# Kernel tuning notes

Measured on AMD Instinct MI355X. Metric: run time of the kernel, lower is better.

## Reference

```python
import jax, jax.numpy as jnp
import numpy as np

N = 50000   # nodes
E = 600000  # edges (avg degree 12)
D = 128     # embedding dim (hardcoded in original: np.zeros(128))
P = 5       # propagation iterations (self.p)


def setup_inputs() -> dict:
    key = jax.random.key(0)
    ks = jax.random.split(key, 10)
    x = jax.random.normal(ks[0], (N, D), jnp.float32)
    g = jax.random.normal(ks[1], (D,), jnp.float32)
    dist = jax.random.uniform(ks[2], (E,), jnp.float32)
    w1 = jax.random.normal(ks[3], (1,), jnp.float32)
    w2 = jax.random.normal(ks[4], (1,), jnp.float32)
    w3 = jax.random.normal(ks[5], (1,), jnp.float32)
    w4 = jax.random.normal(ks[6], (1,), jnp.float32)
    w5 = jax.random.normal(ks[7], (1,), jnp.float32)
    src = jax.random.randint(ks[8], (E,), 0, N)
    dst = jax.random.randint(ks[9], (E,), 0, N)
    return {"x": x, "g": g, "dist": dist, "w1": w1, "w2": w2, "w3": w3,
            "w4": w4, "w5": w5, "src": src, "dst": dst}


def reference(x, g, dist, w1, w2, w3, w4, w5, src, dst):
    # travel_times[i] = sum_{j in N(i)} w5 * dist(i,j)  -- iteration-invariant
    travel = jax.ops.segment_sum(w5[0] * dist, src, num_segments=N)  # [N]
    # per-node affine part, constant across the P iterations
    base = w1[0] * x + w2[0] * g[None, :] + w4[0] * jax.nn.relu(travel)[:, None]  # [N, D]
    u = x  # new_u_vect starts as a copy of x
    for _ in range(P):
        # u_sum[i] = sum_{j in N(i)} u[j]  (gather + segment-sum, synchronous update)
        u_sum = jax.ops.segment_sum(u[dst], src, num_segments=N)  # [N, D]
        u = base + w3[0] * u_sum
    return jax.nn.relu(u)
```

## Files before the change

kernel.cpp:

```cpp
#include <hip/hip_runtime.h>

#define D 128
#define D4 32
#define CAPH 32

typedef float v4f __attribute__((ext_vector_type(4)));
typedef _Float16 h4 __attribute__((ext_vector_type(4)));

static inline size_t align_up(size_t v, size_t a) { return (v + a - 1) & ~(a - 1); }

__global__ void fill_ell_kernel(const int* __restrict__ src,
                                const int* __restrict__ dst,
                                const float* __restrict__ dist,
                                unsigned long long* __restrict__ packedA,
                                unsigned long long* __restrict__ packedB,
                                unsigned short* __restrict__ adjA,
                                unsigned short* __restrict__ adjB,
                                int E, int Ehalf) {
  int e = blockIdx.x * blockDim.x + threadIdx.x;
  if (e >= E) return;
  int s = src[e];
  unsigned long long fx = (unsigned long long)(dist[e] * 4294967296.0f);
  unsigned long long val = (1ull << 48) | fx;
  if (e < Ehalf) {
    unsigned long long old = atomicAdd(&packedA[s], val);
    unsigned int slot = (unsigned int)(old >> 48);
    if (slot < CAPH) adjA[(size_t)s * CAPH + slot] = (unsigned short)dst[e];
  } else {
    unsigned long long old = atomicAdd(&packedB[s], val);
    unsigned int slot = (unsigned int)(old >> 48);
    if (slot < CAPH) adjB[(size_t)s * CAPH + slot] = (unsigned short)dst[e];
  }
}

__global__ void base_seed_kernel(const v4f* __restrict__ x4, const v4f* __restrict__ g4,
                                 const unsigned long long* __restrict__ packedA,
                                 const unsigned long long* __restrict__ packedB,
                                 const float* __restrict__ w1p, const float* __restrict__ w2p,
                                 const float* __restrict__ w4p, const float* __restrict__ w5p,
                                 h4* __restrict__ base, h4* __restrict__ uA,
                                 h4* __restrict__ uB, int n) {
  int i = blockIdx.x * blockDim.x + threadIdx.x;
  int node = i >> 5;
  int lane = i & 31;
  if (node > n) return;
  size_t idx = (size_t)i;
  if (node == n) {
    h4 z = {0, 0, 0, 0};
    uA[idx] = z;
    uB[idx] = z;
    return;
  }
  v4f xv = x4[(size_t)node * D4 + lane];
  v4f gv = g4[lane];
  unsigned long long sum = (packedA[node] & 0xFFFFFFFFFFFFull)
                         + (packedB[node] & 0xFFFFFFFFFFFFull);
  float ds = (float)sum * (1.0f / 4294967296.0f);
  float t = w5p[0] * ds;
  t = t > 0.f ? t : 0.f;
  v4f b = w1p[0] * xv + w2p[0] * gv;
  b += t * w4p[0];
  base[idx] = __builtin_convertvector(b, h4);
  uA[idx] = __builtin_convertvector(xv, h4);
}

__global__ __launch_bounds__(256) void prop_kernel(
    const h4* __restrict__ uin, const h4* __restrict__ base,
    const unsigned long long* __restrict__ packedA,
    const unsigned long long* __restrict__ packedB,
    const unsigned short* __restrict__ adjA,
    const unsigned short* __restrict__ adjB,
    const float* __restrict__ w3p,
    void* __restrict__ uout, int n, int final_relu)
{
  int half  = blockIdx.x & 1;
  int chunk = blockIdx.x >> 1;
  int group = threadIdx.x >> 4;
  int lane  = threadIdx.x & 15;
  int node  = chunk * 16 + group;
  if (node >= n) return;

  unsigned long long pA = packedA[node];
  unsigned long long pB = packedB[node];
  int degA = (int)(pA >> 48); if (degA > CAPH) degA = CAPH;
  int degB = (int)(pB >> 48); if (degB > CAPH) degB = CAPH;

  const unsigned short* rowA = adjA + (size_t)node * CAPH;
  const unsigned short* rowB = adjB + (size_t)node * CAPH;
  int a0 = rowA[lane];
  int a1 = rowA[lane + 16];
  int b0 = rowB[lane];
  int b1 = rowB[lane + 16];

  const h4* uh = uin + (size_t)half * 16 + lane;

  v4f acc0 = {0.f,0.f,0.f,0.f}, acc1 = acc0, acc2 = acc0, acc3 = acc0;

  for (int k = 0; k < degA; k += 8) {
    int sel = (k >= 16) ? a1 : a0;
    int j0 = __shfl(sel, (k + 0) & 15, 16); j0 = (k + 0 < degA) ? j0 : n;
    int j1 = __shfl(sel, (k + 1) & 15, 16); j1 = (k + 1 < degA) ? j1 : n;
    int j2 = __shfl(sel, (k + 2) & 15, 16); j2 = (k + 2 < degA) ? j2 : n;
    int j3 = __shfl(sel, (k + 3) & 15, 16); j3 = (k + 3 < degA) ? j3 : n;
    int j4 = __shfl(sel, (k + 4) & 15, 16); j4 = (k + 4 < degA) ? j4 : n;
    int j5 = __shfl(sel, (k + 5) & 15, 16); j5 = (k + 5 < degA) ? j5 : n;
    int j6 = __shfl(sel, (k + 6) & 15, 16); j6 = (k + 6 < degA) ? j6 : n;
    int j7 = __shfl(sel, (k + 7) & 15, 16); j7 = (k + 7 < degA) ? j7 : n;
    h4 v0 = uh[(size_t)j0 * 32];
    h4 v1 = uh[(size_t)j1 * 32];
    h4 v2 = uh[(size_t)j2 * 32];
    h4 v3 = uh[(size_t)j3 * 32];
    h4 v4 = uh[(size_t)j4 * 32];
    h4 v5 = uh[(size_t)j5 * 32];
    h4 v6 = uh[(size_t)j6 * 32];
    h4 v7 = uh[(size_t)j7 * 32];
    acc0 += __builtin_convertvector(v0, v4f) + __builtin_convertvector(v1, v4f);
    acc1 += __builtin_convertvector(v2, v4f) + __builtin_convertvector(v3, v4f);
    acc2 += __builtin_convertvector(v4, v4f) + __builtin_convertvector(v5, v4f);
    acc3 += __builtin_convertvector(v6, v4f) + __builtin_convertvector(v7, v4f);
  }
  for (int k = 0; k < degB; k += 8) {
    int sel = (k >= 16) ? b1 : b0;
    int j0 = __shfl(sel, (k + 0) & 15, 16); j0 = (k + 0 < degB) ? j0 : n;
    int j1 = __shfl(sel, (k + 1) & 15, 16); j1 = (k + 1 < degB) ? j1 : n;
    int j2 = __shfl(sel, (k + 2) & 15, 16); j2 = (k + 2 < degB) ? j2 : n;
    int j3 = __shfl(sel, (k + 3) & 15, 16); j3 = (k + 3 < degB) ? j3 : n;
    int j4 = __shfl(sel, (k + 4) & 15, 16); j4 = (k + 4 < degB) ? j4 : n;
    int j5 = __shfl(sel, (k + 5) & 15, 16); j5 = (k + 5 < degB) ? j5 : n;
    int j6 = __shfl(sel, (k + 6) & 15, 16); j6 = (k + 6 < degB) ? j6 : n;
    int j7 = __shfl(sel, (k + 7) & 15, 16); j7 = (k + 7 < degB) ? j7 : n;
    h4 v0 = uh[(size_t)j0 * 32];
    h4 v1 = uh[(size_t)j1 * 32];
    h4 v2 = uh[(size_t)j2 * 32];
    h4 v3 = uh[(size_t)j3 * 32];
    h4 v4 = uh[(size_t)j4 * 32];
    h4 v5 = uh[(size_t)j5 * 32];
    h4 v6 = uh[(size_t)j6 * 32];
    h4 v7 = uh[(size_t)j7 * 32];
    acc0 += __builtin_convertvector(v0, v4f) + __builtin_convertvector(v1, v4f);
    acc1 += __builtin_convertvector(v2, v4f) + __builtin_convertvector(v3, v4f);
    acc2 += __builtin_convertvector(v4, v4f) + __builtin_convertvector(v5, v4f);
    acc3 += __builtin_convertvector(v6, v4f) + __builtin_convertvector(v7, v4f);
  }
  v4f asum = (acc0 + acc1) + (acc2 + acc3);

  size_t idx = (size_t)node * 32 + half * 16 + lane;
  v4f bb = __builtin_convertvector(base[idx], v4f);
  v4f r = bb + w3p[0] * asum;

  if (final_relu) {
    r.x = r.x > 0.f ? r.x : 0.f;
    r.y = r.y > 0.f ? r.y : 0.f;
    r.z = r.z > 0.f ? r.z : 0.f;
    r.w = r.w > 0.f ? r.w : 0.f;
    __builtin_nontemporal_store(r, (v4f*)uout + idx);
  } else {
    ((h4*)uout)[idx] = __builtin_convertvector(r, h4);
  }
}

extern "C" void kernel_launch(void* const* d_in, const int* in_sizes, int n_in,
                              void* d_out, int out_size, void* d_ws, size_t ws_size,
                              hipStream_t stream) {
  const float* x    = (const float*)d_in[0];
  const float* g    = (const float*)d_in[1];
  const float* dist = (const float*)d_in[2];
  const float* w1   = (const float*)d_in[3];
  const float* w2   = (const float*)d_in[4];
  const float* w3   = (const float*)d_in[5];
  const float* w4   = (const float*)d_in[6];
  const float* w5   = (const float*)d_in[7];
  const int*   src  = (const int*)d_in[8];
  const int*   dst  = (const int*)d_in[9];

  const int N = in_sizes[0] / D;
  const int E = in_sizes[2];
  const int Ehalf = E / 2;

  char* ws = (char*)d_ws;
  size_t o = 0;
  unsigned long long* packedA = (unsigned long long*)(ws + o); o += align_up((size_t)N * 8, 256);
  unsigned long long* packedB = (unsigned long long*)(ws + o);
  size_t zero_end = o + (size_t)N * 8;
  o += align_up((size_t)N * 8, 256);
  unsigned short* adjA = (unsigned short*)(ws + o); o += align_up((size_t)N * CAPH * 2, 256);
  unsigned short* adjB = (unsigned short*)(ws + o); o += align_up((size_t)N * CAPH * 2, 256);
  h4* baseB = (h4*)(ws + o); o += align_up((size_t)(N + 1) * D * 2, 256);
  h4* uA    = (h4*)(ws + o); o += align_up((size_t)(N + 1) * D * 2, 256);
  h4* uB    = (h4*)(ws + o); o += align_up((size_t)(N + 1) * D * 2, 256);
  float* out = (float*)d_out;

  hipMemsetAsync(ws, 0, zero_end, stream);

  const int tb = 256;
  const int eblocks = (E + tb - 1) / tb;
  const int sthreads = (N + 1) * 32;
  const int sblocks = (sthreads + tb - 1) / tb;

  fill_ell_kernel<<<eblocks, tb, 0, stream>>>(src, dst, dist, packedA, packedB,
                                              adjA, adjB, E, Ehalf);
  base_seed_kernel<<<sblocks, tb, 0, stream>>>((const v4f*)x, (const v4f*)g,
                                               packedA, packedB,
                                               w1, w2, w4, w5, baseB, uA, uB, N);

  const int chunks = (N + 15) / 16;
  const int pblocks = chunks * 2;
  prop_kernel<<<pblocks, 256, 0, stream>>>(uA, baseB, packedA, packedB, adjA, adjB, w3, uB,  N, 0);
  prop_kernel<<<pblocks, 256, 0, stream>>>(uB, baseB, packedA, packedB, adjA, adjB, w3, uA,  N, 0);
  prop_kernel<<<pblocks, 256, 0, stream>>>(uA, baseB, packedA, packedB, adjA, adjB, w3, uB,  N, 0);
  prop_kernel<<<pblocks, 256, 0, stream>>>(uB, baseB, packedA, packedB, adjA, adjB, w3, uA,  N, 0);
  prop_kernel<<<pblocks, 256, 0, stream>>>(uA, baseB, packedA, packedB, adjA, adjB, w3, out, N, 1);
}
```

Measured before the change: 254.3 us.

## Split fp16 node features into four column-quarter planes for gather locality

Stores u and base as four separate planes of 32 columns (64 bytes per node per plane) instead of row-major, and has each block handle one quarter for 32 nodes with 8 lanes per node. Each gather now touches a smaller contiguous slice, and each plane's working set is a quarter of the full array, so it may stay in cache across the blocks that share a quarter. The first 8 neighbors of both edge halves are also peeled into one batch of 16 independent loads to raise memory-level parallelism. The risk is that 64-byte gather segments underuse cache lines, and four times as many blocks each re-read adjacency and degree data.

```diff
diff --git a/kernel.cpp b/kernel.cpp
--- a/kernel.cpp
+++ b/kernel.cpp
@@ -42,17 +42,19 @@
                                  h4* __restrict__ uB, int n) {
   int i = blockIdx.x * blockDim.x + threadIdx.x;
   int node = i >> 5;
-  int lane = i & 31;
+  int l = i & 31;
   if (node > n) return;
-  size_t idx = (size_t)i;
+  int q  = l >> 3;
+  int lq = l & 7;
+  size_t po = ((size_t)q * (n + 1) + node) * 8 + lq;
   if (node == n) {
     h4 z = {0, 0, 0, 0};
-    uA[idx] = z;
-    uB[idx] = z;
+    uA[po] = z;
+    uB[po] = z;
     return;
   }
-  v4f xv = x4[(size_t)node * D4 + lane];
-  v4f gv = g4[lane];
+  v4f xv = x4[(size_t)node * D4 + l];
+  v4f gv = g4[l];
   unsigned long long sum = (packedA[node] & 0xFFFFFFFFFFFFull)
                          + (packedB[node] & 0xFFFFFFFFFFFFull);
   float ds = (float)sum * (1.0f / 4294967296.0f);
@@ -60,8 +62,8 @@
   t = t > 0.f ? t : 0.f;
   v4f b = w1p[0] * xv + w2p[0] * gv;
   b += t * w4p[0];
-  base[idx] = __builtin_convertvector(b, h4);
-  uA[idx] = __builtin_convertvector(xv, h4);
+  base[po] = __builtin_convertvector(b, h4);
+  uA[po]   = __builtin_convertvector(xv, h4);
 }
 
 __global__ __launch_bounds__(256) void prop_kernel(
@@ -73,11 +75,11 @@
     const float* __restrict__ w3p,
     void* __restrict__ uout, int n, int final_relu)
 {
-  int half  = blockIdx.x & 1;
-  int chunk = blockIdx.x >> 1;
-  int group = threadIdx.x >> 4;
-  int lane  = threadIdx.x & 15;
-  int node  = chunk * 16 + group;
+  int q     = blockIdx.x & 3;
+  int chunk = blockIdx.x >> 2;
+  int group = threadIdx.x >> 3;
+  int lane  = threadIdx.x & 7;
+  int node  = chunk * 32 + group;
   if (node >= n) return;
 
   unsigned long long pA = packedA[node];
@@ -88,64 +90,111 @@
   const unsigned short* rowA = adjA + (size_t)node * CAPH;
   const unsigned short* rowB = adjB + (size_t)node * CAPH;
   int a0 = rowA[lane];
-  int a1 = rowA[lane + 16];
+  int a1 = rowA[lane + 8];
+  int a2 = rowA[lane + 16];
+  int a3 = rowA[lane + 24];
   int b0 = rowB[lane];
-  int b1 = rowB[lane + 16];
-
-  const h4* uh = uin + (size_t)half * 16 + lane;
+  int b1 = rowB[lane + 8];
+  int b2 = rowB[lane + 16];
+  int b3 = rowB[lane + 24];
+
+  const h4* uq = uin + ((size_t)q * (n + 1)) * 8 + lane;
+  size_t po = ((size_t)q * (n + 1) + node) * 8 + lane;
+  v4f bb = __builtin_convertvector(base[po], v4f);
 
   v4f acc0 = {0.f,0.f,0.f,0.f}, acc1 = acc0, acc2 = acc0, acc3 = acc0;
 
-  for (int k = 0; k < degA; k += 8) {
-    int sel = (k >= 16) ? a1 : a0;
-    int j0 = __shfl(sel, (k + 0) & 15, 16); j0 = (k + 0 < degA) ? j0 : n;
-    int j1 = __shfl(sel, (k + 1) & 15, 16); j1 = (k + 1 < degA) ? j1 : n;
-    int j2 = __shfl(sel, (k + 2) & 15, 16); j2 = (k + 2 < degA) ? j2 : n;
-    int j3 = __shfl(sel, (k + 3) & 15, 16); j3 = (k + 3 < degA) ? j3 : n;
-    int j4 = __shfl(sel, (k + 4) & 15, 16); j4 = (k + 4 < degA) ? j4 : n;
-    int j5 = __shfl(sel, (k + 5) & 15, 16); j5 = (k + 5 < degA) ? j5 : n;
-    int j6 = __shfl(sel, (k + 6) & 15, 16); j6 = (k + 6 < degA) ? j6 : n;
-    int j7 = __shfl(sel, (k + 7) & 15, 16); j7 = (k + 7 < degA) ? j7 : n;
-    h4 v0 = uh[(size_t)j0 * 32];
-    h4 v1 = uh[(size_t)j1 * 32];
-    h4 v2 = uh[(size_t)j2 * 32];
-    h4 v3 = uh[(size_t)j3 * 32];
-    h4 v4 = uh[(size_t)j4 * 32];
-    h4 v5 = uh[(size_t)j5 * 32];
-    h4 v6 = uh[(size_t)j6 * 32];
-    h4 v7 = uh[(size_t)j7 * 32];
+  {
+    int jA0 = __shfl(a0, 0, 8); jA0 = (0 < degA) ? jA0 : n;
+    int jA1 = __shfl(a0, 1, 8); jA1 = (1 < degA) ? jA1 : n;
+    int jA2 = __shfl(a0, 2, 8); jA2 = (2 < degA) ? jA2 : n;
+    int jA3 = __shfl(a0, 3, 8); jA3 = (3 < degA) ? jA3 : n;
+    int jA4 = __shfl(a0, 4, 8); jA4 = (4 < degA) ? jA4 : n;
+    int jA5 = __shfl(a0, 5, 8); jA5 = (5 < degA) ? jA5 : n;
+    int jA6 = __shfl(a0, 6, 8); jA6 = (6 < degA) ? jA6 : n;
+    int jA7 = __shfl(a0, 7, 8); jA7 = (7 < degA) ? jA7 : n;
+    int jB0 = __shfl(b0, 0, 8); jB0 = (0 < degB) ? jB0 : n;
+    int jB1 = __shfl(b0, 1, 8); jB1 = (1 < degB) ? jB1 : n;
+    int jB2 = __shfl(b0, 2, 8); jB2 = (2 < degB) ? jB2 : n;
+    int jB3 = __shfl(b0, 3, 8); jB3 = (3 < degB) ? jB3 : n;
+    int jB4 = __shfl(b0, 4, 8); jB4 = (4 < degB) ? jB4 : n;
+    int jB5 = __shfl(b0, 5, 8); jB5 = (5 < degB) ? jB5 : n;
+    int jB6 = __shfl(b0, 6, 8); jB6 = (6 < degB) ? jB6 : n;
+    int jB7 = __shfl(b0, 7, 8); jB7 = (7 < degB) ? jB7 : n;
+    h4 vA0 = uq[(size_t)jA0 * 8];
+    h4 vA1 = uq[(size_t)jA1 * 8];
+    h4 vA2 = uq[(size_t)jA2 * 8];
+    h4 vA3 = uq[(size_t)jA3 * 8];
+    h4 vA4 = uq[(size_t)jA4 * 8];
+    h4 vA5 = uq[(size_t)jA5 * 8];
+    h4 vA6 = uq[(size_t)jA6 * 8];
+    h4 vA7 = uq[(size_t)jA7 * 8];
+    h4 vB0 = uq[(size_t)jB0 * 8];
+    h4 vB1 = uq[(size_t)jB1 * 8];
+    h4 vB2 = uq[(size_t)jB2 * 8];
+    h4 vB3 = uq[(size_t)jB3 * 8];
+    h4 vB4 = uq[(size_t)jB4 * 8];
+    h4 vB5 = uq[(size_t)jB5 * 8];
+    h4 vB6 = uq[(size_t)jB6 * 8];
+    h4 vB7 = uq[(size_t)jB7 * 8];
+    acc0 += __builtin_convertvector(vA0, v4f) + __builtin_convertvector(vA1, v4f);
+    acc1 += __builtin_convertvector(vA2, v4f) + __builtin_convertvector(vA3, v4f);
+    acc2 += __builtin_convertvector(vA4, v4f) + __builtin_convertvector(vA5, v4f);
+    acc3 += __builtin_convertvector(vA6, v4f) + __builtin_convertvector(vA7, v4f);
+    acc0 += __builtin_convertvector(vB0, v4f) + __builtin_convertvector(vB1, v4f);
+    acc1 += __builtin_convertvector(vB2, v4f) + __builtin_convertvector(vB3, v4f);
+    acc2 += __builtin_convertvector(vB4, v4f) + __builtin_convertvector(vB5, v4f);
+    acc3 += __builtin_convertvector(vB6, v4f) + __builtin_convertvector(vB7, v4f);
+  }
+
+  for (int k = 8; k < degA; k += 8) {
+    int sel = (k >= 24) ? a3 : (k >= 16) ? a2 : a1;
+    int j0 = __shfl(sel, 0, 8); j0 = (k + 0 < degA) ? j0 : n;
+    int j1 = __shfl(sel, 1, 8); j1 = (k + 1 < degA) ? j1 : n;
+    int j2 = __shfl(sel, 2, 8); j2 = (k + 2 < degA) ? j2 : n;
+    int j3 = __shfl(sel, 3, 8); j3 = (k + 3 < degA) ? j3 : n;
+    int j4 = __shfl(sel, 4, 8); j4 = (k + 4 < degA) ? j4 : n;
+    int j5 = __shfl(sel, 5, 8); j5 = (k + 5 < degA) ? j5 : n;
+    int j6 = __shfl(sel, 6, 8); j6 = (k + 6 < degA) ? j6 : n;
+    int j7 = __shfl(sel, 7, 8); j7 = (k + 7 < degA) ? j7 : n;
+    h4 v0 = uq[(size_t)j0 * 8];
+    h4 v1 = uq[(size_t)j1 * 8];
+    h4 v2 = uq[(size_t)j2 * 8];
+    h4 v3 = uq[(size_t)j3 * 8];
+    h4 v4 = uq[(size_t)j4 * 8];
+    h4 v5 = uq[(size_t)j5 * 8];
+    h4 v6 = uq[(size_t)j6 * 8];
+    h4 v7 = uq[(size_t)j7 * 8];
     acc0 += __builtin_convertvector(v0, v4f) + __builtin_convertvector(v1, v4f);
     acc1 += __builtin_convertvector(v2, v4f) + __builtin_convertvector(v3, v4f);
     acc2 += __builtin_convertvector(v4, v4f) + __builtin_convertvector(v5, v4f);
     acc3 += __builtin_convertvector(v6, v4f) + __builtin_convertvector(v7, v4f);
   }
-  for (int k = 0; k < degB; k += 8) {
-    int sel = (k >= 16) ? b1 : b0;
-    int j0 = __shfl(sel, (k + 0) & 15, 16); j0 = (k + 0 < degB) ? j0 : n;
-    int j1 = __shfl(sel, (k + 1) & 15, 16); j1 = (k + 1 < degB) ? j1 : n;
-    int j2 = __shfl(sel, (k + 2) & 15, 16); j2 = (k + 2 < degB) ? j2 : n;
-    int j3 = __shfl(sel, (k + 3) & 15, 16); j3 = (k + 3 < degB) ? j3 : n;
-    int j4 = __shfl(sel, (k + 4) & 15, 16); j4 = (k + 4 < degB) ? j4 : n;
-    int j5 = __shfl(sel, (k + 5) & 15, 16); j5 = (k + 5 < degB) ? j5 : n;
-    int j6 = __shfl(sel, (k + 6) & 15, 16); j6 = (k + 6 < degB) ? j6 : n;
-    int j7 = __shfl(sel, (k + 7) & 15, 16); j7 = (k + 7 < degB) ? j7 : n;
-    h4 v0 = uh[(size_t)j0 * 32];
-    h4 v1 = uh[(size_t)j1 * 32];
-    h4 v2 = uh[(size_t)j2 * 32];
-    h4 v3 = uh[(size_t)j3 * 32];
-    h4 v4 = uh[(size_t)j4 * 32];
-    h4 v5 = uh[(size_t)j5 * 32];
-    h4 v6 = uh[(size_t)j6 * 32];
-    h4 v7 = uh[(size_t)j7 * 32];
+  for (int k = 8; k < degB; k += 8) {
+    int sel = (k >= 24) ? b3 : (k >= 16) ? b2 : b1;
+    int j0 = __shfl(sel, 0, 8); j0 = (k + 0 < degB) ? j0 : n;
+    int j1 = __shfl(sel, 1, 8); j1 = (k + 1 < degB) ? j1 : n;
+    int j2 = __shfl(sel, 2, 8); j2 = (k + 2 < degB) ? j2 : n;
+    int j3 = __shfl(sel, 3, 8); j3 = (k + 3 < degB) ? j3 : n;
+    int j4 = __shfl(sel, 4, 8); j4 = (k + 4 < degB) ? j4 : n;
+    int j5 = __shfl(sel, 5, 8); j5 = (k + 5 < degB) ? j5 : n;
+    int j6 = __shfl(sel, 6, 8); j6 = (k + 6 < degB) ? j6 : n;
+    int j7 = __shfl(sel, 7, 8); j7 = (k + 7 < degB) ? j7 : n;
+    h4 v0 = uq[(size_t)j0 * 8];
+    h4 v1 = uq[(size_t)j1 * 8];
+    h4 v2 = uq[(size_t)j2 * 8];
+    h4 v3 = uq[(size_t)j3 * 8];
+    h4 v4 = uq[(size_t)j4 * 8];
+    h4 v5 = uq[(size_t)j5 * 8];
+    h4 v6 = uq[(size_t)j6 * 8];
+    h4 v7 = uq[(size_t)j7 * 8];
     acc0 += __builtin_convertvector(v0, v4f) + __builtin_convertvector(v1, v4f);
     acc1 += __builtin_convertvector(v2, v4f) + __builtin_convertvector(v3, v4f);
     acc2 += __builtin_convertvector(v4, v4f) + __builtin_convertvector(v5, v4f);
     acc3 += __builtin_convertvector(v6, v4f) + __builtin_convertvector(v7, v4f);
   }
+
   v4f asum = (acc0 + acc1) + (acc2 + acc3);
-
-  size_t idx = (size_t)node * 32 + half * 16 + lane;
-  v4f bb = __builtin_convertvector(base[idx], v4f);
   v4f r = bb + w3p[0] * asum;
 
   if (final_relu) {
@@ -153,9 +202,9 @@
     r.y = r.y > 0.f ? r.y : 0.f;
     r.z = r.z > 0.f ? r.z : 0.f;
     r.w = r.w > 0.f ? r.w : 0.f;
-    __builtin_nontemporal_store(r, (v4f*)uout + idx);
+    __builtin_nontemporal_store(r, (v4f*)uout + (size_t)node * 32 + q * 8 + lane);
   } else {
-    ((h4*)uout)[idx] = __builtin_convertvector(r, h4);
+    ((h4*)uout)[po] = __builtin_convertvector(r, h4);
   }
 }
 
@@ -203,8 +252,8 @@
                                                packedA, packedB,
                                                w1, w2, w4, w5, baseB, uA, uB, N);
 
-  const int chunks = (N + 15) / 16;
-  const int pblocks = chunks * 2;
+  const int chunks = (N + 31) / 32;
+  const int pblocks = chunks * 4;
   prop_kernel<<<pblocks, 256, 0, stream>>>(uA, baseB, packedA, packedB, adjA, adjB, w3, uB,  N, 0);
   prop_kernel<<<pblocks, 256, 0, stream>>>(uB, baseB, packedA, packedB, adjA, adjB, w3, uA,  N, 0);
   prop_kernel<<<pblocks, 256, 0, stream>>>(uA, baseB, packedA, packedB, adjA, adjB, w3, uB,  N, 0);
```

Result: slower. 272.5 us (+7.2%).
